# Kernel optimization log

Measured on AMD Instinct MI355X. Metric: run time of the kernel, lower is better.

Reference implementation:

```python
import jax, jax.numpy as jnp
import numpy as np
import math

NUM_HEADS = 16
HEAD_DIM = 64
DIM = 1024
IO_SLOTS = 16
NEG_INF = 1.0e9


def _alibi_slopes(num_heads):
    # slopes = ratio**i for i in 1..n, ratio = 2**(-8/n)
    ratio = 2.0 ** (-8.0 / num_heads)
    return jnp.array([ratio ** i for i in range(1, num_heads + 1)], dtype=jnp.float32)


def setup_inputs() -> dict:
    key = jax.random.key(0)
    ks = jax.random.split(key, 7)
    B, S, D = 2, 2048, DIM
    x = jax.random.normal(ks[0], (B, S, D), dtype=jnp.float32)
    is_getchar = jax.random.uniform(ks[1], (B, S), dtype=jnp.float32)
    is_putchar = jax.random.uniform(ks[2], (B, S), dtype=jnp.float32)
    scale = 0.02
    wq = jax.random.normal(ks[3], (D, NUM_HEADS * HEAD_DIM), dtype=jnp.float32) * scale
    wk = jax.random.normal(ks[4], (D, NUM_HEADS * HEAD_DIM), dtype=jnp.float32) * scale
    wv = jax.random.normal(ks[5], (D, NUM_HEADS * HEAD_DIM), dtype=jnp.float32) * scale
    wo = jax.random.normal(ks[6], (NUM_HEADS * HEAD_DIM, D), dtype=jnp.float32) * scale
    return {"x": x, "is_getchar": is_getchar, "is_putchar": is_putchar,
            "wq": wq, "wk": wk, "wv": wv, "wo": wo}


def reference(x, is_getchar, is_putchar, wq, wk, wv, wo):
    B, S, D = x.shape
    H, hd = NUM_HEADS, HEAD_DIM
    io_start = D - IO_SLOTS

    q = (x @ wq).reshape(B, S, H, hd)
    k = (x @ wk).reshape(B, S, H, hd)
    v = (x @ wv).reshape(B, S, H, hd)

    # scores[b,h,i,j] = q . k / sqrt(hd)
    scores = jnp.einsum("bihd,bjhd->bhij", q, k) / math.sqrt(hd)

    # standard ALiBi bias: -slope * (i - j), causal masked
    positions = jnp.arange(S)
    dist = (positions[:, None] - positions[None, :]).astype(jnp.float32)  # [S,S] = i - j
    slopes = _alibi_slopes(H)  # [H]
    bias = -slopes[:, None, None] * dist  # [H,S,S]
    causal = jnp.triu(jnp.ones((S, S), dtype=jnp.float32), k=1)
    bias = bias - causal * NEG_INF
    scores = scores + bias[None]

    # targeted read-head bias on head 0: -slope0 * |target - j|
    read_anchor = x[..., io_start + 0]  # [B,S]
    read_offset = x[..., io_start + 1]  # [B,S]
    target = read_anchor + 1.0 + read_offset  # [B,S]
    read_bias = -slopes[0] * jnp.abs(target[..., None] - positions.astype(jnp.float32))  # [B,S,S]
    head0 = jnp.where(is_getchar[:, None, :, None] > 0.5, read_bias[:, None], scores[:, :1])
    scores = scores.at[:, :1].set(head0)

    attn = jax.nn.softmax(scores, axis=-1)
    attn_out = jnp.einsum("bhij,bjhd->bihd", attn, v).reshape(B, S, H * hd)
    output = x + attn_out @ wo

    # I/O state updates (last 16 channels)
    output = output.at[..., io_start + 1].add(is_getchar)   # read_offset += getchar
    output = output.at[..., io_start + 3].add(is_putchar)   # write_offset += putchar
    output = output.at[..., io_start + 13].set(is_putchar)  # output_ready = putchar
    return output
```

## Files before the change

kernel.cpp:

```cpp
#include <hip/hip_runtime.h>
#include <hip/hip_bf16.h>

typedef __hip_bfloat16 bf16;
typedef __attribute__((ext_vector_type(8))) short short8;
typedef __attribute__((ext_vector_type(4))) short short4v;
typedef __attribute__((ext_vector_type(4))) float f32x4;

#define MFMA16(a, b, c) __builtin_amdgcn_mfma_f32_16x16x32_bf16((a), (b), (c), 0, 0, 0)

#if __has_builtin(__builtin_amdgcn_mfma_f32_16x16x16bf16_1k)
#define MFMA_PV(a, b, c) __builtin_amdgcn_mfma_f32_16x16x16bf16_1k((a), (b), (c), 0, 0, 0)
#elif __has_builtin(__builtin_amdgcn_mfma_f32_16x16x16_bf16)
#define MFMA_PV(a, b, c) __builtin_amdgcn_mfma_f32_16x16x16_bf16((a), (b), (c), 0, 0, 0)
#else
static __device__ __forceinline__ f32x4 mfma_pv_asm(short4v a, short4v b, f32x4 c) {
    f32x4 d;
    asm volatile("v_mfma_f32_16x16x16_bf16 %0, %1, %2, %3"
                 : "=&v"(d) : "v"(a), "v"(b), "v"(c));
    return d;
}
#define MFMA_PV(a, b, c) mfma_pv_asm((a), (b), (c))
#endif

static __device__ __forceinline__ void gload_lds16(const bf16* g, bf16* l) {
    __builtin_amdgcn_global_load_lds((const __attribute__((address_space(1))) void*)g,
                                     (__attribute__((address_space(3))) void*)l, 16, 0, 0);
}

__global__ __launch_bounds__(256) void cast_x_kernel(const float* __restrict__ in,
                                                     bf16* __restrict__ out) {
    int i = (blockIdx.x * 256 + threadIdx.x) * 4;
    float4 v = *(const float4*)(in + i);
    union { bf16 h4[4]; uint2 u; } p;
    p.h4[0] = __float2bfloat16(v.x);
    p.h4[1] = __float2bfloat16(v.y);
    p.h4[2] = __float2bfloat16(v.z);
    p.h4[3] = __float2bfloat16(v.w);
    *(uint2*)(out + i) = p.u;
}

__global__ __launch_bounds__(256) void transpose_cast_kernel(
    const float* __restrict__ wq, const float* __restrict__ wk,
    const float* __restrict__ wv, const float* __restrict__ wo,
    bf16* __restrict__ WqkvT, bf16* __restrict__ WoT) {
    __shared__ bf16 tile[64][65];
    int bid = blockIdx.x;
    int mat = bid >> 8;
    int t   = bid & 255;
    int tn  = t >> 4, tk = t & 15;
    const float* src = (mat == 0) ? wq : (mat == 1) ? wk : (mat == 2) ? wv : wo;
    bf16* dst = (mat < 3) ? (WqkvT + (size_t)mat * 1024 * 1024) : WoT;
    int tx = threadIdx.x & 63, ty = threadIdx.x >> 6;
    int k0 = tk * 64, n0 = tn * 64;
#pragma unroll
    for (int p = 0; p < 16; ++p) {
        int r = p * 4 + ty;
        tile[r][tx] = __float2bfloat16(src[(size_t)(k0 + r) * 1024 + n0 + tx]);
    }
    __syncthreads();
#pragma unroll
    for (int p = 0; p < 16; ++p) {
        int r = p * 4 + ty;
        dst[(size_t)(n0 + r) * 1024 + k0 + tx] = tile[tx][r];
    }
}

__global__ __launch_bounds__(256) void gemm_qkv_kernel(
    const bf16* __restrict__ A, const bf16* __restrict__ Bt,
    bf16* __restrict__ QK, bf16* __restrict__ Vt) {
    const int K = 1024;
    int bm = blockIdx.x, bn = blockIdx.y;
    __shared__ bf16 As[128 * 32];
    __shared__ bf16 Bs[128 * 32];
    int tid = threadIdx.x;
    int lane = tid & 63, w = tid >> 6;
    int wm = (w >> 1) * 64, wn = (w & 1) * 64;
    int q4 = lane >> 4, li = lane & 15;
    int srow = tid >> 2, sc = (tid & 3) * 8;

    const bf16* Ag = A + (size_t)(bm * 128 + srow) * K + sc;
    const bf16* Bg = Bt + (size_t)(bn * 128 + srow) * K + sc;
    bf16* Asl = As + tid * 8;
    bf16* Asl2 = As + 2048 + tid * 8;
    bf16* Bsl = Bs + tid * 8;
    bf16* Bsl2 = Bs + 2048 + tid * 8;

    f32x4 acc[4][4];
#pragma unroll
    for (int mt = 0; mt < 4; ++mt)
#pragma unroll
        for (int nt = 0; nt < 4; ++nt) acc[mt][nt] = (f32x4){0.f, 0.f, 0.f, 0.f};

    for (int k0 = 0; k0 < K; k0 += 32) {
        __syncthreads();
        gload_lds16(Ag + k0, Asl);
        gload_lds16(Ag + 64 * K + k0, Asl2);
        gload_lds16(Bg + k0, Bsl);
        gload_lds16(Bg + 64 * K + k0, Bsl2);
        __syncthreads();
        short8 af[4], bfb[4];
#pragma unroll
        for (int mt = 0; mt < 4; ++mt)
            af[mt] = *(const short8*)(As + (wm + mt * 16 + li) * 32 + q4 * 8);
#pragma unroll
        for (int nt = 0; nt < 4; ++nt)
            bfb[nt] = *(const short8*)(Bs + (wn + nt * 16 + li) * 32 + q4 * 8);
#pragma unroll
        for (int mt = 0; mt < 4; ++mt)
#pragma unroll
            for (int nt = 0; nt < 4; ++nt)
                acc[mt][nt] = MFMA16(af[mt], bfb[nt], acc[mt][nt]);
    }

    int rowb = bm * 128 + wm;
    if (bn < 16) {
#pragma unroll
        for (int mt = 0; mt < 4; ++mt) {
#pragma unroll
            for (int nt = 0; nt < 4; ++nt) {
                int col = bn * 128 + wn + nt * 16 + li;
#pragma unroll
                for (int r = 0; r < 4; ++r) {
                    int row = rowb + mt * 16 + q4 * 4 + r;
                    QK[(size_t)row * 2048 + col] = __float2bfloat16(acc[mt][nt][r]);
                }
            }
        }
    } else {
#pragma unroll
        for (int mt = 0; mt < 4; ++mt) {
            int sbase = rowb + mt * 16 + q4 * 4;
            int b = sbase >> 11, s = sbase & 2047;
#pragma unroll
            for (int nt = 0; nt < 4; ++nt) {
                int n = bn * 128 + wn + nt * 16 + li - 2048;
                int h = n >> 6, d = n & 63;
                union { bf16 h4[4]; uint2 u; } pk;
#pragma unroll
                for (int r = 0; r < 4; ++r) pk.h4[r] = __float2bfloat16(acc[mt][nt][r]);
                *(uint2*)(Vt + (size_t)((b * 16 + h) * 64 + d) * 2048 + s) = pk.u;
            }
        }
    }
}

__global__ __launch_bounds__(256, 3) void attn_kernel(
    const bf16* __restrict__ QK, const bf16* __restrict__ Vt,
    const float* __restrict__ x, const float* __restrict__ gch,
    bf16* __restrict__ AO) {
    const int S = 2048;
    int idx = blockIdx.x;
    int ti, h, b;
    if (idx < 64) { h = 0; b = idx & 1; ti = idx >> 1; }
    else {
        int i2 = idx - 64;
        int row = i2 / 30;
        int j = i2 - row * 30;
        ti = 31 - row; h = 1 + (j >> 1); b = j & 1;
    }
    int i0 = ti * 64;
    int tid = threadIdx.x, lane = tid & 63, w = tid >> 6;
    int q4 = lane >> 4, li = lane & 15;

    __shared__ __align__(16) char smem[36864];
    bf16* KsB = (bf16*)smem;
    bf16* VsB = (bf16*)(smem + 18432);
    float* Ored = (float*)smem;
    float* lsumBuf = (float*)(smem + 17408);

    short8 qf[4][2];
#pragma unroll
    for (int it = 0; it < 4; ++it) {
        const bf16* qp = QK + (size_t)(b * S + i0 + it * 16 + li) * 2048 + h * 64 + q4 * 8;
        qf[it][0] = *(const short8*)(qp);
        qf[it][1] = *(const short8*)(qp + 32);
    }

    const float L2E = 1.4426950408889634f;
    float slope = exp2f(-0.5f * (float)(h + 1));
    float s1  = 0.125f * L2E;
    float sl1 = slope * L2E;
    const float slope0_1 = 0.70710678118654752f * L2E;

    float tgt[4]; int gcm[4];
    if (h == 0) {
#pragma unroll
        for (int it = 0; it < 4; ++it) {
            size_t ix = (size_t)(b * S + i0 + it * 16 + li);
            gcm[it] = gch[ix] > 0.5f ? 1 : 0;
            tgt[it] = x[ix * 1024 + 1008] + 1.0f + x[ix * 1024 + 1009];
        }
    } else {
#pragma unroll
        for (int it = 0; it < 4; ++it) { gcm[it] = 0; tgt[it] = 0.f; }
    }

    float lsum[4] = {0.f, 0.f, 0.f, 0.f};
    f32x4 o[4][4];
#pragma unroll
    for (int it = 0; it < 4; ++it)
#pragma unroll
        for (int dt = 0; dt < 4; ++dt) o[it][dt] = (f32x4){0.f, 0.f, 0.f, 0.f};

    int srow = tid >> 3, scv = (tid & 7) * 8;
    const bf16* Kg = QK + (size_t)(b * S + srow) * 2048 + 1024 + h * 64 + scv;
    const bf16* Vg = Vt + (size_t)((b * 16 + h) * 64 + srow) * 2048 + scv;

    int ntiles = (h == 0) ? (S / 64) : (ti + 1);

    {
        uint4 kv0 = *(const uint4*)(Kg);
        uint4 kv1 = *(const uint4*)(Kg + (size_t)32 * 2048);
        uint4 vv0 = *(const uint4*)(Vg);
        uint4 vv1 = *(const uint4*)(Vg + (size_t)32 * 2048);
        *(uint4*)(KsB + srow * 72 + scv) = kv0;
        *(uint4*)(KsB + (srow + 32) * 72 + scv) = kv1;
        *(uint4*)(VsB + srow * 72 + scv) = vv0;
        *(uint4*)(VsB + (srow + 32) * 72 + scv) = vv1;
    }
    __syncthreads();

    int cur = 0;
    for (int jt = 0; jt < ntiles; ++jt) {
        int j0 = jt * 64;
        uint4 nk0, nk1, nv0, nv1;
        bool pref = (jt + 1 < ntiles);
        if (pref) {
            int jn = j0 + 64;
            nk0 = *(const uint4*)(Kg + (size_t)jn * 2048);
            nk1 = *(const uint4*)(Kg + (size_t)(jn + 32) * 2048);
            nv0 = *(const uint4*)(Vg + jn);
            nv1 = *(const uint4*)(Vg + (size_t)32 * 2048 + jn);
        }
        const bf16* Ks = KsB + cur * 4608;
        const bf16* Vs = VsB + cur * 4608;

        short8 kf0 = *(const short8*)(Ks + (w * 16 + li) * 72 + q4 * 8);
        short8 kf1 = *(const short8*)(Ks + (w * 16 + li) * 72 + 32 + q4 * 8);
        f32x4 sAcc[4];
#pragma unroll
        for (int it = 0; it < 4; ++it) {
            f32x4 z = (f32x4){0.f, 0.f, 0.f, 0.f};
            z = MFMA16(kf0, qf[it][0], z);
            z = MFMA16(kf1, qf[it][1], z);
            sAcc[it] = z;
        }

        float jbase = (float)(j0 + w * 16 + q4 * 4);
        int maskable = (jt >= ti);
        short4v pf[4];
#pragma unroll
        for (int it = 0; it < 4; ++it) {
            float fi = (float)(i0 + it * 16 + li);
            float d0 = jbase - fi;
            union { bf16 hh[4]; short4v v; } pu;
#pragma unroll
            for (int r = 0; r < 4; ++r) {
                float dj = d0 + (float)r;
                float s = fmaf(sl1, dj, sAcc[it][r] * s1);
                float p;
                if (h == 0) {
                    float jj = jbase + (float)r;
                    float sg = -slope0_1 * fabsf(tgt[it] - jj);
                    s = gcm[it] ? sg : s;
                    bool msk = (!gcm[it]) && (dj > 0.f);
                    p = msk ? 0.f : exp2f(s);
                } else {
                    p = exp2f(s);
                    if (maskable && dj > 0.f) p = 0.f;
                }
                lsum[it] += p;
                pu.hh[r] = __float2bfloat16(p);
            }
            pf[it] = pu.v;
        }

#pragma unroll
        for (int dt = 0; dt < 4; ++dt) {
            short4v vf = *(const short4v*)(Vs + (dt * 16 + li) * 72 + w * 16 + q4 * 4);
#pragma unroll
            for (int it = 0; it < 4; ++it)
                o[it][dt] = MFMA_PV(pf[it], vf, o[it][dt]);
        }

        if (pref) {
            bf16* Kn = KsB + (cur ^ 1) * 4608;
            bf16* Vn = VsB + (cur ^ 1) * 4608;
            *(uint4*)(Kn + srow * 72 + scv) = nk0;
            *(uint4*)(Kn + (srow + 32) * 72 + scv) = nk1;
            *(uint4*)(Vn + srow * 72 + scv) = nv0;
            *(uint4*)(Vn + (srow + 32) * 72 + scv) = nv1;
        }
        __syncthreads();
        cur ^= 1;
    }

#pragma unroll
    for (int it = 0; it < 4; ++it) {
        lsum[it] += __shfl_xor(lsum[it], 16, 64);
        lsum[it] += __shfl_xor(lsum[it], 32, 64);
    }
    if (lane < 16) {
#pragma unroll
        for (int it = 0; it < 4; ++it) lsumBuf[w * 64 + it * 16 + lane] = lsum[it];
    }

    __syncthreads();
    if (w == 0) {
#pragma unroll
        for (int it = 0; it < 4; ++it)
#pragma unroll
            for (int dt = 0; dt < 4; ++dt)
#pragma unroll
                for (int r = 0; r < 4; ++r)
                    Ored[(it * 16 + q4 * 4 + r) * 68 + dt * 16 + li] = o[it][dt][r];
    }
    __syncthreads();
    if (w == 1) {
#pragma unroll
        for (int it = 0; it < 4; ++it)
#pragma unroll
            for (int dt = 0; dt < 4; ++dt)
#pragma unroll
                for (int r = 0; r < 4; ++r)
                    Ored[(it * 16 + q4 * 4 + r) * 68 + dt * 16 + li] += o[it][dt][r];
    }
    __syncthreads();
    if (w == 2) {
#pragma unroll
        for (int it = 0; it < 4; ++it)
#pragma unroll
            for (int dt = 0; dt < 4; ++dt)
#pragma unroll
                for (int r = 0; r < 4; ++r)
                    Ored[(it * 16 + q4 * 4 + r) * 68 + dt * 16 + li] += o[it][dt][r];
    }
    __syncthreads();
    if (w == 3) {
#pragma unroll
        for (int it = 0; it < 4; ++it)
#pragma unroll
            for (int dt = 0; dt < 4; ++dt)
#pragma unroll
                for (int r = 0; r < 4; ++r)
                    Ored[(it * 16 + q4 * 4 + r) * 68 + dt * 16 + li] += o[it][dt][r];
    }
    __syncthreads();

    int i = tid >> 2, dseg = (tid & 3) * 16;
    float ls = lsumBuf[0 * 64 + i] + lsumBuf[1 * 64 + i] + lsumBuf[2 * 64 + i] + lsumBuf[3 * 64 + i];
    float inv = 1.0f / ls;
    bf16* dst = AO + (size_t)(b * S + i0 + i) * 1024 + h * 64 + dseg;
    union { bf16 hh[16]; uint4 u[2]; } ou;
#pragma unroll
    for (int c = 0; c < 16; ++c)
        ou.hh[c] = __float2bfloat16(Ored[i * 68 + dseg + c] * inv);
    *(uint4*)(dst) = ou.u[0];
    *(uint4*)(dst + 8) = ou.u[1];
}

__global__ __launch_bounds__(256) void gemm_out_kernel(
    const bf16* __restrict__ A, const bf16* __restrict__ Bt,
    const float* __restrict__ x, float* __restrict__ out,
    const float* __restrict__ gch, const float* __restrict__ pch) {
    const int K = 1024;
    int bm = blockIdx.x, bn = blockIdx.y;
    __shared__ bf16 As[128 * 32];
    __shared__ bf16 Bs[128 * 32];
    int tid = threadIdx.x;
    int lane = tid & 63, w = tid >> 6;
    int wm = (w >> 1) * 64, wn = (w & 1) * 64;
    int q4 = lane >> 4, li = lane & 15;
    int srow = tid >> 2, sc = (tid & 3) * 8;

    const bf16* Ag = A + (size_t)(bm * 128 + srow) * K + sc;
    const bf16* Bg = Bt + (size_t)(bn * 128 + srow) * K + sc;
    bf16* Asl = As + tid * 8;
    bf16* Asl2 = As + 2048 + tid * 8;
    bf16* Bsl = Bs + tid * 8;
    bf16* Bsl2 = Bs + 2048 + tid * 8;

    f32x4 acc[4][4];
#pragma unroll
    for (int mt = 0; mt < 4; ++mt)
#pragma unroll
        for (int nt = 0; nt < 4; ++nt) acc[mt][nt] = (f32x4){0.f, 0.f, 0.f, 0.f};

    for (int k0 = 0; k0 < K; k0 += 32) {
        __syncthreads();
        gload_lds16(Ag + k0, Asl);
        gload_lds16(Ag + 64 * K + k0, Asl2);
        gload_lds16(Bg + k0, Bsl);
        gload_lds16(Bg + 64 * K + k0, Bsl2);
        __syncthreads();
        short8 af[4], bfb[4];
#pragma unroll
        for (int mt = 0; mt < 4; ++mt)
            af[mt] = *(const short8*)(As + (wm + mt * 16 + li) * 32 + q4 * 8);
#pragma unroll
        for (int nt = 0; nt < 4; ++nt)
            bfb[nt] = *(const short8*)(Bs + (wn + nt * 16 + li) * 32 + q4 * 8);
#pragma unroll
        for (int mt = 0; mt < 4; ++mt)
#pragma unroll
            for (int nt = 0; nt < 4; ++nt)
                acc[mt][nt] = MFMA16(af[mt], bfb[nt], acc[mt][nt]);
    }

#pragma unroll
    for (int mt = 0; mt < 4; ++mt) {
#pragma unroll
        for (int nt = 0; nt < 4; ++nt) {
            int col = bn * 128 + wn + nt * 16 + li;
#pragma unroll
            for (int r = 0; r < 4; ++r) {
                int row = bm * 128 + wm + mt * 16 + q4 * 4 + r;
                size_t idx = (size_t)row * 1024 + col;
                float v = x[idx] + acc[mt][nt][r];
                if (col == 1009) v += gch[row];
                else if (col == 1011) v += pch[row];
                else if (col == 1021) v = pch[row];
                out[idx] = v;
            }
        }
    }
}

extern "C" void kernel_launch(void* const* d_in, const int* in_sizes, int n_in,
                              void* d_out, int out_size, void* d_ws, size_t ws_size,
                              hipStream_t stream) {
    (void)in_sizes; (void)n_in; (void)out_size; (void)ws_size;
    const float* x   = (const float*)d_in[0];
    const float* gch = (const float*)d_in[1];
    const float* pch = (const float*)d_in[2];
    const float* wq  = (const float*)d_in[3];
    const float* wk  = (const float*)d_in[4];
    const float* wv  = (const float*)d_in[5];
    const float* wo  = (const float*)d_in[6];
    float* out = (float*)d_out;

    char* ws = (char*)d_ws;
    bf16* Xb    = (bf16*)(ws);
    bf16* WqkvT = (bf16*)(ws + (size_t)( 8 << 20));
    bf16* WoT   = (bf16*)(ws + (size_t)(14 << 20));
    bf16* QK    = (bf16*)(ws + (size_t)(16 << 20));
    bf16* Vt    = (bf16*)(ws + (size_t)(32 << 20));
    bf16* AO    = Xb;

    cast_x_kernel<<<4096, 256, 0, stream>>>(x, Xb);
    transpose_cast_kernel<<<1024, 256, 0, stream>>>(wq, wk, wv, wo, WqkvT, WoT);
    gemm_qkv_kernel<<<dim3(32, 24), 256, 0, stream>>>(Xb, WqkvT, QK, Vt);
    attn_kernel<<<1024, 256, 0, stream>>>(QK, Vt, x, gch, AO);
    gemm_out_kernel<<<dim3(32, 8), 256, 0, stream>>>(AO, WoT, x, out, gch, pch);
}
```

Before: 208.1 us.

## Rewrite QKV GEMM with 256x192 tiles, 4-stage LDS pipeline and swizzle

Rewrites the QKV projection GEMM to use 512-thread blocks computing 256x192 output tiles on a 16x16 grid, which is 256 blocks instead of 768. Global-to-LDS loads now run through a 4-slot ring buffer with explicit vmcnt waits and split barriers, so the next stages are prefetched while the MFMAs run. LDS rows are XOR-swizzled to avoid bank conflicts, and s_setprio is raised around the MFMA bursts. The goal is to hide memory latency and raise per-block reuse, at the cost of fragile hand-counted waits, about 112KB of LDS per block, and a wave tile that straddles the Q/K and V output boundary.

```diff
diff --git a/kernel.cpp b/kernel.cpp
--- a/kernel.cpp
+++ b/kernel.cpp
@@ -65,83 +65,137 @@
     }
 }
 
-__global__ __launch_bounds__(256) void gemm_qkv_kernel(
+__global__ __launch_bounds__(512, 2) void gemm_qkv_kernel(
     const bf16* __restrict__ A, const bf16* __restrict__ Bt,
     bf16* __restrict__ QK, bf16* __restrict__ Vt) {
     const int K = 1024;
     int bm = blockIdx.x, bn = blockIdx.y;
-    __shared__ bf16 As[128 * 32];
-    __shared__ bf16 Bs[128 * 32];
     int tid = threadIdx.x;
     int lane = tid & 63, w = tid >> 6;
-    int wm = (w >> 1) * 64, wn = (w & 1) * 64;
     int q4 = lane >> 4, li = lane & 15;
-    int srow = tid >> 2, sc = (tid & 3) * 8;
-
-    const bf16* Ag = A + (size_t)(bm * 128 + srow) * K + sc;
-    const bf16* Bg = Bt + (size_t)(bn * 128 + srow) * K + sc;
-    bf16* Asl = As + tid * 8;
-    bf16* Asl2 = As + 2048 + tid * 8;
-    bf16* Bsl = Bs + tid * 8;
-    bf16* Bsl2 = Bs + 2048 + tid * 8;
-
-    f32x4 acc[4][4];
-#pragma unroll
-    for (int mt = 0; mt < 4; ++mt)
-#pragma unroll
-        for (int nt = 0; nt < 4; ++nt) acc[mt][nt] = (f32x4){0.f, 0.f, 0.f, 0.f};
-
-    for (int k0 = 0; k0 < K; k0 += 32) {
-        __syncthreads();
-        gload_lds16(Ag + k0, Asl);
-        gload_lds16(Ag + 64 * K + k0, Asl2);
-        gload_lds16(Bg + k0, Bsl);
-        gload_lds16(Bg + 64 * K + k0, Bsl2);
-        __syncthreads();
-        short8 af[4], bfb[4];
-#pragma unroll
-        for (int mt = 0; mt < 4; ++mt)
-            af[mt] = *(const short8*)(As + (wm + mt * 16 + li) * 32 + q4 * 8);
-#pragma unroll
-        for (int nt = 0; nt < 4; ++nt)
-            bfb[nt] = *(const short8*)(Bs + (wn + nt * 16 + li) * 32 + q4 * 8);
-#pragma unroll
-        for (int mt = 0; mt < 4; ++mt)
-#pragma unroll
-            for (int nt = 0; nt < 4; ++nt)
-                acc[mt][nt] = MFMA16(af[mt], bfb[nt], acc[mt][nt]);
-    }
-
-    int rowb = bm * 128 + wm;
-    if (bn < 16) {
-#pragma unroll
-        for (int mt = 0; mt < 4; ++mt) {
-#pragma unroll
-            for (int nt = 0; nt < 4; ++nt) {
-                int col = bn * 128 + wn + nt * 16 + li;
-#pragma unroll
-                for (int r = 0; r < 4; ++r) {
-                    int row = rowb + mt * 16 + q4 * 4 + r;
-                    QK[(size_t)row * 2048 + col] = __float2bfloat16(acc[mt][nt][r]);
-                }
+    int wm = (w >> 2) * 128;
+    int wn = (w & 3) * 48;
+
+    __shared__ __align__(16) bf16 smem[4 * 14336];
+
+    int rA = tid >> 2, cA = tid & 3;
+    int tB = tid & 255;
+    int rB1 = 128 + (tB >> 2), cB1 = tB & 3;
+    int swA0 = ((cA ^ (rA & 3)) << 3);
+    int swA1 = ((cA ^ ((128 + rA) & 3)) << 3);
+    int swB0 = swA0;
+    int swB1 = ((cB1 ^ (rB1 & 3)) << 3);
+    const bf16* Ag0 = A + (size_t)(bm * 256 + rA) * K + swA0;
+    const bf16* Ag1 = A + (size_t)(bm * 256 + 128 + rA) * K + swA1;
+    const bf16* Bg0 = Bt + (size_t)(bn * 192 + rB1 - 128 + (tB >> 2) - (tB >> 2)) * K;
+    const bf16* Bgp0 = Bt + (size_t)(bn * 192 + (tid >> 2)) * K + ((cA ^ ((tid >> 2) & 3)) << 3);
+    const bf16* Bgp1 = Bt + (size_t)(bn * 192 + rB1) * K + swB1;
+    (void)Bg0;
+
+    int dA0 = tid * 8;
+    int dA1 = 4096 + tid * 8;
+    int dB0 = 8192 + tid * 8;
+    int dB1 = 8192 + 4096 + tB * 8;
+
+    f32x4 acc[8][3];
+#pragma unroll
+    for (int mt = 0; mt < 8; ++mt)
+#pragma unroll
+        for (int nt = 0; nt < 3; ++nt) acc[mt][nt] = (f32x4){0.f, 0.f, 0.f, 0.f};
+
+#define STAGE_A(slot, s_) do { \
+        bf16* sl = smem + (slot) * 14336; \
+        gload_lds16(Ag0 + (s_) * 32, sl + dA0); \
+        gload_lds16(Ag1 + (s_) * 32, sl + dA1); } while (0)
+#define STAGE_B(slot, s_) do { \
+        bf16* sl = smem + (slot) * 14336; \
+        gload_lds16(Bgp0 + (s_) * 32, sl + dB0); \
+        gload_lds16(Bgp1 + (s_) * 32, sl + dB1); } while (0)
+
+    STAGE_A(0, 0); STAGE_B(0, 0);
+    STAGE_A(1, 1); STAGE_B(1, 1);
+    STAGE_A(2, 2); STAGE_B(2, 2);
+    asm volatile("s_waitcnt vmcnt(8)" ::: "memory");
+    __builtin_amdgcn_s_barrier();
+
+#define AFRAG(sl, mt_) (*(const short8*)((sl) + (wm + (mt_) * 16 + li) * 32 + ((q4 ^ ((wm + (mt_) * 16 + li) & 3)) << 3)))
+#define BFRAG(sl, nt_) (*(const short8*)((sl) + 8192 + (wn + (nt_) * 16 + li) * 32 + ((q4 ^ ((wn + (nt_) * 16 + li) & 3)) << 3)))
+
+    for (int s = 0; s < 32; ++s) {
+        const bf16* sl = smem + (s & 3) * 14336;
+        int sn = s + 3;
+        int slotn = sn & 3;
+        bool st = (sn < 32);
+
+        short8 a0 = AFRAG(sl, 0), a1 = AFRAG(sl, 1), a2 = AFRAG(sl, 2), a3 = AFRAG(sl, 3);
+        short8 b0 = BFRAG(sl, 0), b1 = BFRAG(sl, 1), b2 = BFRAG(sl, 2);
+        if (st) STAGE_A(slotn, sn);
+        __builtin_amdgcn_s_barrier();
+        __builtin_amdgcn_s_setprio(1);
+        acc[0][0] = MFMA16(a0, b0, acc[0][0]);
+        acc[0][1] = MFMA16(a0, b1, acc[0][1]);
+        acc[0][2] = MFMA16(a0, b2, acc[0][2]);
+        acc[1][0] = MFMA16(a1, b0, acc[1][0]);
+        acc[1][1] = MFMA16(a1, b1, acc[1][1]);
+        acc[1][2] = MFMA16(a1, b2, acc[1][2]);
+        acc[2][0] = MFMA16(a2, b0, acc[2][0]);
+        acc[2][1] = MFMA16(a2, b1, acc[2][1]);
+        acc[2][2] = MFMA16(a2, b2, acc[2][2]);
+        acc[3][0] = MFMA16(a3, b0, acc[3][0]);
+        acc[3][1] = MFMA16(a3, b1, acc[3][1]);
+        acc[3][2] = MFMA16(a3, b2, acc[3][2]);
+        __builtin_amdgcn_s_setprio(0);
+        __builtin_amdgcn_s_barrier();
+
+        short8 a4 = AFRAG(sl, 4), a5 = AFRAG(sl, 5), a6 = AFRAG(sl, 6), a7 = AFRAG(sl, 7);
+        if (st) STAGE_B(slotn, sn);
+        __builtin_amdgcn_s_barrier();
+        __builtin_amdgcn_s_setprio(1);
+        acc[4][0] = MFMA16(a4, b0, acc[4][0]);
+        acc[4][1] = MFMA16(a4, b1, acc[4][1]);
+        acc[4][2] = MFMA16(a4, b2, acc[4][2]);
+        acc[5][0] = MFMA16(a5, b0, acc[5][0]);
+        acc[5][1] = MFMA16(a5, b1, acc[5][1]);
+        acc[5][2] = MFMA16(a5, b2, acc[5][2]);
+        acc[6][0] = MFMA16(a6, b0, acc[6][0]);
+        acc[6][1] = MFMA16(a6, b1, acc[6][1]);
+        acc[6][2] = MFMA16(a6, b2, acc[6][2]);
+        acc[7][0] = MFMA16(a7, b0, acc[7][0]);
+        acc[7][1] = MFMA16(a7, b1, acc[7][1]);
+        acc[7][2] = MFMA16(a7, b2, acc[7][2]);
+        __builtin_amdgcn_s_setprio(0);
+
+        if (s < 29)       asm volatile("s_waitcnt vmcnt(8)" ::: "memory");
+        else if (s == 29) asm volatile("s_waitcnt vmcnt(4)" ::: "memory");
+        else              asm volatile("s_waitcnt vmcnt(0)" ::: "memory");
+        __builtin_amdgcn_s_barrier();
+    }
+
+#pragma unroll
+    for (int mt = 0; mt < 8; ++mt) {
+        int rowb = bm * 256 + wm + mt * 16 + q4 * 4;
+#pragma unroll
+        for (int nt = 0; nt < 3; ++nt) {
+            int col = bn * 192 + wn + nt * 16 + li;
+            if (col < 2048) {
+#pragma unroll
+                for (int r = 0; r < 4; ++r)
+                    QK[(size_t)(rowb + r) * 2048 + col] = __float2bfloat16(acc[mt][nt][r]);
+            } else {
+                int n2 = col - 2048;
+                int h = n2 >> 6, d = n2 & 63;
+                int bb = rowb >> 11, ss = rowb & 2047;
+                union { bf16 h4[4]; uint2 u; } pk;
+#pragma unroll
+                for (int r = 0; r < 4; ++r) pk.h4[r] = __float2bfloat16(acc[mt][nt][r]);
+                *(uint2*)(Vt + (size_t)((bb * 16 + h) * 64 + d) * 2048 + ss) = pk.u;
             }
         }
-    } else {
-#pragma unroll
-        for (int mt = 0; mt < 4; ++mt) {
-            int sbase = rowb + mt * 16 + q4 * 4;
-            int b = sbase >> 11, s = sbase & 2047;
-#pragma unroll
-            for (int nt = 0; nt < 4; ++nt) {
-                int n = bn * 128 + wn + nt * 16 + li - 2048;
-                int h = n >> 6, d = n & 63;
-                union { bf16 h4[4]; uint2 u; } pk;
-#pragma unroll
-                for (int r = 0; r < 4; ++r) pk.h4[r] = __float2bfloat16(acc[mt][nt][r]);
-                *(uint2*)(Vt + (size_t)((b * 16 + h) * 64 + d) * 2048 + s) = pk.u;
-            }
-        }
-    }
+    }
+#undef STAGE_A
+#undef STAGE_B
+#undef AFRAG
+#undef BFRAG
 }
 
 __global__ __launch_bounds__(256, 3) void attn_kernel(
@@ -449,7 +503,7 @@
 
     cast_x_kernel<<<4096, 256, 0, stream>>>(x, Xb);
     transpose_cast_kernel<<<1024, 256, 0, stream>>>(wq, wk, wv, wo, WqkvT, WoT);
-    gemm_qkv_kernel<<<dim3(32, 24), 256, 0, stream>>>(Xb, WqkvT, QK, Vt);
+    gemm_qkv_kernel<<<dim3(16, 16), 512, 0, stream>>>(Xb, WqkvT, QK, Vt);
     attn_kernel<<<1024, 256, 0, stream>>>(QK, Vt, x, gch, AO);
     gemm_out_kernel<<<dim3(32, 8), 256, 0, stream>>>(AO, WoT, x, out, gch, pch);
 }
```

After: 210.6 us. About the same (+1.2%).

## Split long attention KV ranges across two blocks and combine partials

Applied to the files above, without the earlier changes.

Query tiles with long key ranges (head 0 and the later causal rows, ti>=16) now have their KV loop split into two halves, each handled by its own block. Each half writes unnormalized fp32 partial outputs and row sums to workspace, and a new combine kernel adds the two and normalizes into AO. This shortens the critical path of the longest blocks and improves load balance across CUs. The cost is an extra launch plus fp32 partial traffic. The partials can simply be summed because ALiBi with a causal mask keeps scores bounded and the kernel uses no running max.

```diff
diff --git a/kernel.cpp b/kernel.cpp
--- a/kernel.cpp
+++ b/kernel.cpp
@@ -144,19 +144,28 @@
     }
 }
 
-__global__ __launch_bounds__(256, 3) void attn_kernel(
+__global__ __launch_bounds__(256, 3) void attn_part_kernel(
     const bf16* __restrict__ QK, const bf16* __restrict__ Vt,
     const float* __restrict__ x, const float* __restrict__ gch,
-    bf16* __restrict__ AO) {
+    bf16* __restrict__ AO, float* __restrict__ Opart, float* __restrict__ lpart) {
     const int S = 2048;
     int idx = blockIdx.x;
-    int ti, h, b;
-    if (idx < 64) { h = 0; b = idx & 1; ti = idx >> 1; }
-    else {
-        int i2 = idx - 64;
-        int row = i2 / 30;
-        int j = i2 - row * 30;
-        ti = 31 - row; h = 1 + (j >> 1); b = j & 1;
+    int ti, h, b, jlo, jhi, split;
+    if (idx < 128) {
+        split = 1; h = 0; int part = idx & 1; b = (idx >> 1) & 1; ti = idx >> 2;
+        jlo = part * 16; jhi = jlo + 16;
+    } else if (idx < 1088) {
+        split = 1; int i2 = idx - 128;
+        int row = i2 / 60; int j = i2 - row * 60;
+        ti = 31 - row; int hb = j >> 1; int part = j & 1;
+        h = 1 + (hb >> 1); b = hb & 1;
+        int nt = ti + 1, half = (nt + 1) >> 1;
+        jlo = part ? half : 0; jhi = part ? nt : half;
+    } else {
+        split = 0; int i3 = idx - 1088;
+        int row = i3 / 30; int j = i3 - row * 30;
+        ti = 15 - row; h = 1 + (j >> 1); b = j & 1;
+        jlo = 0; jhi = ti + 1;
     }
     int i0 = ti * 64;
     int tid = threadIdx.x, lane = tid & 63, w = tid >> 6;
@@ -206,13 +215,12 @@
     const bf16* Kg = QK + (size_t)(b * S + srow) * 2048 + 1024 + h * 64 + scv;
     const bf16* Vg = Vt + (size_t)((b * 16 + h) * 64 + srow) * 2048 + scv;
 
-    int ntiles = (h == 0) ? (S / 64) : (ti + 1);
-
     {
-        uint4 kv0 = *(const uint4*)(Kg);
-        uint4 kv1 = *(const uint4*)(Kg + (size_t)32 * 2048);
-        uint4 vv0 = *(const uint4*)(Vg);
-        uint4 vv1 = *(const uint4*)(Vg + (size_t)32 * 2048);
+        int j0 = jlo * 64;
+        uint4 kv0 = *(const uint4*)(Kg + (size_t)j0 * 2048);
+        uint4 kv1 = *(const uint4*)(Kg + (size_t)(j0 + 32) * 2048);
+        uint4 vv0 = *(const uint4*)(Vg + j0);
+        uint4 vv1 = *(const uint4*)(Vg + (size_t)32 * 2048 + j0);
         *(uint4*)(KsB + srow * 72 + scv) = kv0;
         *(uint4*)(KsB + (srow + 32) * 72 + scv) = kv1;
         *(uint4*)(VsB + srow * 72 + scv) = vv0;
@@ -221,10 +229,10 @@
     __syncthreads();
 
     int cur = 0;
-    for (int jt = 0; jt < ntiles; ++jt) {
+    for (int jt = jlo; jt < jhi; ++jt) {
         int j0 = jt * 64;
         uint4 nk0, nk1, nv0, nv1;
-        bool pref = (jt + 1 < ntiles);
+        bool pref = (jt + 1 < jhi);
         if (pref) {
             int jn = j0 + 64;
             nk0 = *(const uint4*)(Kg + (size_t)jn * 2048);
@@ -349,12 +357,47 @@
 
     int i = tid >> 2, dseg = (tid & 3) * 16;
     float ls = lsumBuf[0 * 64 + i] + lsumBuf[1 * 64 + i] + lsumBuf[2 * 64 + i] + lsumBuf[3 * 64 + i];
-    float inv = 1.0f / ls;
-    bf16* dst = AO + (size_t)(b * S + i0 + i) * 1024 + h * 64 + dseg;
+    if (split) {
+        float* po = Opart + (size_t)idx * 4096 + i * 64 + dseg;
+#pragma unroll
+        for (int c = 0; c < 16; c += 4)
+            *(float4*)(po + c) = *(const float4*)(&Ored[i * 68 + dseg + c]);
+        if ((tid & 3) == 0) lpart[idx * 64 + i] = ls;
+    } else {
+        float inv = 1.0f / ls;
+        bf16* dst = AO + (size_t)(b * S + i0 + i) * 1024 + h * 64 + dseg;
+        union { bf16 hh[16]; uint4 u[2]; } ou;
+#pragma unroll
+        for (int c = 0; c < 16; ++c)
+            ou.hh[c] = __float2bfloat16(Ored[i * 68 + dseg + c] * inv);
+        *(uint4*)(dst) = ou.u[0];
+        *(uint4*)(dst + 8) = ou.u[1];
+    }
+}
+
+__global__ __launch_bounds__(256) void attn_combine_kernel(
+    const float* __restrict__ Opart, const float* __restrict__ lpart,
+    bf16* __restrict__ AO) {
+    int g = blockIdx.x;
+    int ti, h, b, s0;
+    if (g < 64) { ti = g >> 1; b = g & 1; h = 0; s0 = g * 2; }
+    else {
+        int g2 = g - 64;
+        int row = g2 / 30; int j = g2 - row * 30;
+        ti = 31 - row; h = 1 + (j >> 1); b = j & 1;
+        s0 = 128 + row * 60 + j * 2;
+    }
+    int tid = threadIdx.x;
+    int i = tid >> 2, dseg = (tid & 3) * 16;
+    const float* p0 = Opart + (size_t)s0 * 4096 + i * 64 + dseg;
+    const float* p1 = p0 + 4096;
+    float l = lpart[s0 * 64 + i] + lpart[(s0 + 1) * 64 + i];
+    float inv = 1.0f / l;
     union { bf16 hh[16]; uint4 u[2]; } ou;
 #pragma unroll
     for (int c = 0; c < 16; ++c)
-        ou.hh[c] = __float2bfloat16(Ored[i * 68 + dseg + c] * inv);
+        ou.hh[c] = __float2bfloat16((p0[c] + p1[c]) * inv);
+    bf16* dst = AO + (size_t)(b * 2048 + ti * 64 + i) * 1024 + h * 64 + dseg;
     *(uint4*)(dst) = ou.u[0];
     *(uint4*)(dst + 8) = ou.u[1];
 }
@@ -440,16 +483,19 @@
     float* out = (float*)d_out;
 
     char* ws = (char*)d_ws;
-    bf16* Xb    = (bf16*)(ws);
-    bf16* WqkvT = (bf16*)(ws + (size_t)( 8 << 20));
-    bf16* WoT   = (bf16*)(ws + (size_t)(14 << 20));
-    bf16* QK    = (bf16*)(ws + (size_t)(16 << 20));
-    bf16* Vt    = (bf16*)(ws + (size_t)(32 << 20));
-    bf16* AO    = Xb;
+    bf16* Xb     = (bf16*)(ws);
+    bf16* WqkvT  = (bf16*)(ws + (size_t)( 8 << 20));
+    bf16* WoT    = (bf16*)(ws + (size_t)(14 << 20));
+    bf16* QK     = (bf16*)(ws + (size_t)(16 << 20));
+    bf16* Vt     = (bf16*)(ws + (size_t)(32 << 20));
+    float* Opart = (float*)(ws + (size_t)(40 << 20));
+    float* lpart = (float*)(ws + (size_t)(58 << 20));
+    bf16* AO     = Xb;
 
     cast_x_kernel<<<4096, 256, 0, stream>>>(x, Xb);
     transpose_cast_kernel<<<1024, 256, 0, stream>>>(wq, wk, wv, wo, WqkvT, WoT);
     gemm_qkv_kernel<<<dim3(32, 24), 256, 0, stream>>>(Xb, WqkvT, QK, Vt);
-    attn_kernel<<<1024, 256, 0, stream>>>(QK, Vt, x, gch, AO);
+    attn_part_kernel<<<1568, 256, 0, stream>>>(QK, Vt, x, gch, AO, Opart, lpart);
+    attn_combine_kernel<<<544, 256, 0, stream>>>(Opart, lpart, AO);
     gemm_out_kernel<<<dim3(32, 8), 256, 0, stream>>>(AO, WoT, x, out, gch, pch);
 }
```

Measured after the change: 225.7 us. 1.08x slower.

## Give each wave private K/V LDS buffers and drop per-tile block barriers

Applied to the files above, without the earlier changes.

Each wave only consumes its own 16 keys and the matching 16 V columns per tile, so the shared 64-row K/V double buffers are replaced with per-wave double buffers that each wave loads and reads itself. This removes the block-wide __syncthreads in the main loop and lets the four waves advance independently. A barrier is added before the lsum/Ored reduction because those buffers now alias the per-wave regions. The V tile uses an unpadded 16-element row stride, which may cause LDS bank conflicts, and correctness relies on intra-wave ordering of LDS writes and reads without an explicit fence.

```diff
diff --git a/kernel.cpp b/kernel.cpp
--- a/kernel.cpp
+++ b/kernel.cpp
@@ -162,11 +162,11 @@
     int tid = threadIdx.x, lane = tid & 63, w = tid >> 6;
     int q4 = lane >> 4, li = lane & 15;
 
-    __shared__ __align__(16) char smem[36864];
-    bf16* KsB = (bf16*)smem;
-    bf16* VsB = (bf16*)(smem + 18432);
+    __shared__ __align__(16) char smem[34816];
     float* Ored = (float*)smem;
     float* lsumBuf = (float*)(smem + 17408);
+    bf16* wb0 = (bf16*)(smem + w * 8704);
+    bf16* wb1 = (bf16*)(smem + w * 8704 + 4352);
 
     short8 qf[4][2];
 #pragma unroll
@@ -202,23 +202,24 @@
 #pragma unroll
         for (int dt = 0; dt < 4; ++dt) o[it][dt] = (f32x4){0.f, 0.f, 0.f, 0.f};
 
-    int srow = tid >> 3, scv = (tid & 7) * 8;
-    const bf16* Kg = QK + (size_t)(b * S + srow) * 2048 + 1024 + h * 64 + scv;
-    const bf16* Vg = Vt + (size_t)((b * 16 + h) * 64 + srow) * 2048 + scv;
+    int kR = lane >> 3, kc = (lane & 7) * 8;
+    int vR = lane >> 1, vc = (lane & 1) * 8;
+    const bf16* KgW = QK + (size_t)(b * S + w * 16 + kR) * 2048 + 1024 + h * 64 + kc;
+    const bf16* VgW = Vt + (size_t)((b * 16 + h) * 64 + vR) * 2048 + w * 16 + vc;
 
     int ntiles = (h == 0) ? (S / 64) : (ti + 1);
 
     {
-        uint4 kv0 = *(const uint4*)(Kg);
-        uint4 kv1 = *(const uint4*)(Kg + (size_t)32 * 2048);
-        uint4 vv0 = *(const uint4*)(Vg);
-        uint4 vv1 = *(const uint4*)(Vg + (size_t)32 * 2048);
-        *(uint4*)(KsB + srow * 72 + scv) = kv0;
-        *(uint4*)(KsB + (srow + 32) * 72 + scv) = kv1;
-        *(uint4*)(VsB + srow * 72 + scv) = vv0;
-        *(uint4*)(VsB + (srow + 32) * 72 + scv) = vv1;
-    }
-    __syncthreads();
+        uint4 k0v = *(const uint4*)(KgW);
+        uint4 k1v = *(const uint4*)(KgW + (size_t)8 * 2048);
+        uint4 v0v = *(const uint4*)(VgW);
+        uint4 v1v = *(const uint4*)(VgW + (size_t)32 * 2048);
+        *(uint4*)(wb0 + kR * 72 + kc) = k0v;
+        *(uint4*)(wb0 + (kR + 8) * 72 + kc) = k1v;
+        bf16* vv = wb0 + 16 * 72;
+        *(uint4*)(vv + vR * 16 + vc) = v0v;
+        *(uint4*)(vv + (32 + vR) * 16 + vc) = v1v;
+    }
 
     int cur = 0;
     for (int jt = 0; jt < ntiles; ++jt) {
@@ -227,16 +228,16 @@
         bool pref = (jt + 1 < ntiles);
         if (pref) {
             int jn = j0 + 64;
-            nk0 = *(const uint4*)(Kg + (size_t)jn * 2048);
-            nk1 = *(const uint4*)(Kg + (size_t)(jn + 32) * 2048);
-            nv0 = *(const uint4*)(Vg + jn);
-            nv1 = *(const uint4*)(Vg + (size_t)32 * 2048 + jn);
-        }
-        const bf16* Ks = KsB + cur * 4608;
-        const bf16* Vs = VsB + cur * 4608;
-
-        short8 kf0 = *(const short8*)(Ks + (w * 16 + li) * 72 + q4 * 8);
-        short8 kf1 = *(const short8*)(Ks + (w * 16 + li) * 72 + 32 + q4 * 8);
+            nk0 = *(const uint4*)(KgW + (size_t)jn * 2048);
+            nk1 = *(const uint4*)(KgW + (size_t)(jn + 8) * 2048);
+            nv0 = *(const uint4*)(VgW + jn);
+            nv1 = *(const uint4*)(VgW + (size_t)32 * 2048 + jn);
+        }
+        const bf16* Ks = cur ? wb1 : wb0;
+        const bf16* Vs = Ks + 16 * 72;
+
+        short8 kf0 = *(const short8*)(Ks + li * 72 + q4 * 8);
+        short8 kf1 = *(const short8*)(Ks + li * 72 + 32 + q4 * 8);
         f32x4 sAcc[4];
 #pragma unroll
         for (int it = 0; it < 4; ++it) {
@@ -277,21 +278,20 @@
 
 #pragma unroll
         for (int dt = 0; dt < 4; ++dt) {
-            short4v vf = *(const short4v*)(Vs + (dt * 16 + li) * 72 + w * 16 + q4 * 4);
+            short4v vf = *(const short4v*)(Vs + (dt * 16 + li) * 16 + q4 * 4);
 #pragma unroll
             for (int it = 0; it < 4; ++it)
                 o[it][dt] = MFMA_PV(pf[it], vf, o[it][dt]);
         }
 
         if (pref) {
-            bf16* Kn = KsB + (cur ^ 1) * 4608;
-            bf16* Vn = VsB + (cur ^ 1) * 4608;
-            *(uint4*)(Kn + srow * 72 + scv) = nk0;
-            *(uint4*)(Kn + (srow + 32) * 72 + scv) = nk1;
-            *(uint4*)(Vn + srow * 72 + scv) = nv0;
-            *(uint4*)(Vn + (srow + 32) * 72 + scv) = nv1;
-        }
-        __syncthreads();
+            bf16* Kn = cur ? wb0 : wb1;
+            bf16* Vn = Kn + 16 * 72;
+            *(uint4*)(Kn + kR * 72 + kc) = nk0;
+            *(uint4*)(Kn + (kR + 8) * 72 + kc) = nk1;
+            *(uint4*)(Vn + vR * 16 + vc) = nv0;
+            *(uint4*)(Vn + (32 + vR) * 16 + vc) = nv1;
+        }
         cur ^= 1;
     }
 
@@ -300,6 +300,7 @@
         lsum[it] += __shfl_xor(lsum[it], 16, 64);
         lsum[it] += __shfl_xor(lsum[it], 32, 64);
     }
+    __syncthreads();
     if (lane < 16) {
 #pragma unroll
         for (int it = 0; it < 4; ++it) lsumBuf[w * 64 + it * 16 + lane] = lsum[it];
```

After: 226.1 us. 8.6% more time.
